# Kernel optimization log

Hardware: AMD Instinct MI355X
Metric: run time of the kernel (lower is better)

Reference implementation:

```python
import jax, jax.numpy as jnp
import numpy as np

INPUT, HIDDEN, OUTPUT = 512, 512, 512


def setup_inputs() -> dict:
    key = jax.random.key(0)
    ks = jax.random.split(key, 8)
    B, T = 64, 1024
    s_x = 1.0 / np.sqrt(INPUT)
    s_h = 1.0 / np.sqrt(HIDDEN)
    return {
        "x": jax.random.normal(ks[0], (B, T, INPUT), jnp.float32),
        "h0": jnp.zeros((B, HIDDEN), jnp.float32),
        # nn.Linear params: weight (out, in), bias (out,), U(-1/sqrt(in), 1/sqrt(in))
        "W_xh": jax.random.uniform(ks[1], (HIDDEN, INPUT), jnp.float32, -s_x, s_x),
        "b_xh": jax.random.uniform(ks[2], (HIDDEN,), jnp.float32, -s_x, s_x),
        "W_hh": jax.random.uniform(ks[3], (HIDDEN, HIDDEN), jnp.float32, -s_h, s_h),
        "b_hh": jax.random.uniform(ks[4], (HIDDEN,), jnp.float32, -s_h, s_h),
        "W_hy": jax.random.uniform(ks[5], (OUTPUT, HIDDEN), jnp.float32, -s_h, s_h),
        "b_hy": jax.random.uniform(ks[6], (OUTPUT,), jnp.float32, -s_h, s_h),
    }


def reference(x, h0, W_xh, b_xh, W_hh, b_hh, W_hy, b_hy):
    # h_t = tanh(W_hh h_{t-1} + b_hh + W_xh x_t + b_xh); y_t = W_hy h_t + b_hy
    # Precompute the input projection for all timesteps (one big GEMM).
    xp = jnp.einsum("bti,hi->bth", x, W_xh) + b_xh + b_hh  # (B, T, H)

    def step(h, xp_t):
        h = jnp.tanh(h @ W_hh.T + xp_t)
        return h, h

    h_n, hs = jax.lax.scan(step, h0, jnp.swapaxes(xp, 0, 1))  # hs: (T, B, H)
    hs = jnp.swapaxes(hs, 0, 1)  # (B, T, H)
    output = jnp.einsum("bth,oh->bto", hs, W_hy) + b_hy
    return output, h_n
```

## Files before the change

kernel.cpp:

```cpp
#include <hip/hip_runtime.h>

typedef _Float16 f16;
typedef _Float16 f16x2 __attribute__((ext_vector_type(2)));
typedef _Float16 f16x4 __attribute__((ext_vector_type(4)));
typedef _Float16 f16x8 __attribute__((ext_vector_type(8)));
typedef float    f32x4 __attribute__((ext_vector_type(4)));
typedef int      intx4 __attribute__((ext_vector_type(4)));


__global__ void cvt_f32_to_f16(const float* __restrict__ in, f16* __restrict__ out, int n) {
  int i = (blockIdx.x * blockDim.x + threadIdx.x) * 4;
  if (i + 3 < n) {
    float4 v = *(const float4*)(in + i);
    f16x4 h; h[0] = (f16)v.x; h[1] = (f16)v.y; h[2] = (f16)v.z; h[3] = (f16)v.w;
    *(f16x4*)(out + i) = h;
  }
}

__global__ void bias_comb_kernel(const float* __restrict__ a, const float* __restrict__ b,
                                 float* __restrict__ o, int n) {
  int i = blockIdx.x * blockDim.x + threadIdx.x;
  if (i < n) o[i] = a[i] + b[i];
}

__global__ void zero_u32_kernel(unsigned* p) { *p = 0u; }

__global__ void wabsmax_kernel(const float* __restrict__ in, int n, unsigned* out) {
  float m = 0.f;
  for (int i = blockIdx.x * blockDim.x + threadIdx.x; i < n; i += gridDim.x * blockDim.x)
    m = fmaxf(m, fabsf(in[i]));
#pragma unroll
  for (int off = 32; off >= 1; off >>= 1)
    m = fmaxf(m, __shfl_xor(m, off));
  if ((threadIdx.x & 63) == 0) atomicMax(out, __float_as_uint(m));
}

__global__ void quant_w_kernel(const float* __restrict__ W, signed char* __restrict__ out,
                               const unsigned* __restrict__ wmax, int n) {
  float mx = __uint_as_float(*wmax);
  float inv = mx > 0.f ? 127.f / mx : 0.f;
  int i = (blockIdx.x * blockDim.x + threadIdx.x) * 4;
  if (i + 3 < n) {
    float4 v = *(const float4*)(W + i);
    int q0 = (int)__builtin_rintf(v.x * inv);
    int q1 = (int)__builtin_rintf(v.y * inv);
    int q2 = (int)__builtin_rintf(v.z * inv);
    int q3 = (int)__builtin_rintf(v.w * inv);
    unsigned p = (unsigned)(q0 & 255) | ((unsigned)(q1 & 255) << 8) |
                 ((unsigned)(q2 & 255) << 16) | ((unsigned)(q3 & 255) << 24);
    *(unsigned*)(out + i) = p;
  }
}


#define BM 128
#define BN 128
#define BKT 32
#define LDK 40

template <bool A_IS_F32>
__global__ __launch_bounds__(256, 2) void gemm_f16_kernel(
    const void* __restrict__ Aptr,
    const f16* __restrict__ B,
    const float* __restrict__ bias,
    float* __restrict__ C,
    int M, int N, int K) {
  __shared__ f16 As[BM][LDK];
  __shared__ f16 Bs[BN][LDK];

  const int tid = threadIdx.x;
  const int bm = blockIdx.y, bn = blockIdx.x;
  const int wave = tid >> 6, lane = tid & 63;
  const int wm = wave >> 1, wn = wave & 1;

  f32x4 acc[4][4] = {};

  for (int k0 = 0; k0 < K; k0 += BKT) {
#pragma unroll
    for (int it = 0; it < 2; ++it) {
      int idx = tid + it * 256;
      int row = idx >> 2;
      int kc  = (idx & 3) << 3;
      if (A_IS_F32) {
        const float* Af = (const float*)Aptr + (size_t)(bm * BM + row) * K + k0 + kc;
        float4 v0 = *(const float4*)Af;
        float4 v1 = *(const float4*)(Af + 4);
        f16x8 h;
        h[0] = (f16)v0.x; h[1] = (f16)v0.y; h[2] = (f16)v0.z; h[3] = (f16)v0.w;
        h[4] = (f16)v1.x; h[5] = (f16)v1.y; h[6] = (f16)v1.z; h[7] = (f16)v1.w;
        *(f16x8*)&As[row][kc] = h;
      } else {
        const f16* Ah = (const f16*)Aptr + (size_t)(bm * BM + row) * K + k0 + kc;
        *(f16x8*)&As[row][kc] = *(const f16x8*)Ah;
      }
      const f16* Bh = B + (size_t)(bn * BN + row) * K + k0 + kc;
      *(f16x8*)&Bs[row][kc] = *(const f16x8*)Bh;
    }
    __syncthreads();

    const int fr = lane & 15;
    const int fk = (lane >> 4) << 3;
    f16x8 af[4], bf[4];
#pragma unroll
    for (int i = 0; i < 4; ++i) af[i] = *(const f16x8*)&As[wm * 64 + i * 16 + fr][fk];
#pragma unroll
    for (int j = 0; j < 4; ++j) bf[j] = *(const f16x8*)&Bs[wn * 64 + j * 16 + fr][fk];
#pragma unroll
    for (int i = 0; i < 4; ++i)
#pragma unroll
      for (int j = 0; j < 4; ++j)
        acc[i][j] = __builtin_amdgcn_mfma_f32_16x16x32_f16(af[i], bf[j], acc[i][j], 0, 0, 0);
    __syncthreads();
  }

  const int fr = lane & 15;
  const int fq = lane >> 4;
#pragma unroll
  for (int i = 0; i < 4; ++i)
#pragma unroll
    for (int j = 0; j < 4; ++j)
#pragma unroll
      for (int r = 0; r < 4; ++r) {
        int row = bm * BM + wm * 64 + i * 16 + fq * 4 + r;
        int col = bn * BN + wn * 64 + j * 16 + fr;
        C[(size_t)row * N + col] = acc[i][j][r] + bias[col];
      }
}


#define RT 512

#define MFMA(d, a, b) \
  asm("v_mfma_i32_16x16x64_i8 %0, %1, %2, %0" : "+v"(d) : "v"(a), "a"(b))

#define KSTEP2(s, Aeven, Bt0, Bt1, Bt2, Bt3) { \
    MFMA(Aeven##0, A##s, Bt0);                 \
    MFMA(Aeven##1, A##s, Bt1);                 \
    MFMA(Aeven##2, A##s, Bt2);                 \
    MFMA(Aeven##3, A##s, Bt3); }

#define BLD(s, nt) (*(const intx4*)(Whq + (size_t)(jb + (nt) * 16) * 512 + (s) * 64 + qoff))

__global__ __launch_bounds__(RT, 1) void rnn_scan_kernel(
    const signed char* __restrict__ Whq,
    const unsigned* __restrict__ wmax,
    const float* __restrict__ h0,
    const float* __restrict__ xp,
    f16* __restrict__ hs,
    float* __restrict__ hn,
    int T) {
  __shared__ __align__(64) signed char hbuf[2][RT];
  const int tid  = threadIdx.x;
  const int lane = tid & 63;
  const int w    = tid >> 6;
  const int b    = blockIdx.x;
  const int g    = lane >> 4;
  const int jb   = w * 64 + (lane & 15);
  const int j    = jb + g * 16;
  const int qoff = g << 4;

  const float qs = __uint_as_float(*wmax) * (1.0f / 16129.0f);

  intx4 B0_0=BLD(0,0), B0_1=BLD(0,1), B0_2=BLD(0,2), B0_3=BLD(0,3);
  intx4 B1_0=BLD(1,0), B1_1=BLD(1,1), B1_2=BLD(1,2), B1_3=BLD(1,3);
  intx4 B2_0=BLD(2,0), B2_1=BLD(2,1), B2_2=BLD(2,2), B2_3=BLD(2,3);
  intx4 B3_0=BLD(3,0), B3_1=BLD(3,1), B3_2=BLD(3,2), B3_3=BLD(3,3);
  intx4 B4_0=BLD(4,0), B4_1=BLD(4,1), B4_2=BLD(4,2), B4_3=BLD(4,3);
  intx4 B5_0=BLD(5,0), B5_1=BLD(5,1), B5_2=BLD(5,2), B5_3=BLD(5,3);
  intx4 B6_0=BLD(6,0), B6_1=BLD(6,1), B6_2=BLD(6,2), B6_3=BLD(6,3);
  intx4 B7_0=BLD(7,0), B7_1=BLD(7,1), B7_2=BLD(7,2), B7_3=BLD(7,3);

  {
    float hv = h0[(size_t)b * 512 + tid];
    hv = fminf(1.f, fmaxf(-1.f, hv));
    hbuf[0][tid] = (signed char)(int)__builtin_rintf(127.f * hv);
  }
  __syncthreads();

  const float* xpb = xp + (size_t)b * T * 512 + j;
  f16* hsb = hs + (size_t)b * T * 512 + j;

  int cur = 0;
  float hlast = 0.f;
  float xv = xpb[0];

  for (int t = 0; t < T; ++t) {
    int tn = t + 1 < T ? t + 1 : t;
    float xn = xpb[(size_t)tn * 512];

    const intx4* ap = (const intx4*)(&hbuf[cur][0] + qoff);
    intx4 A0 = ap[0],  A1 = ap[4],  A2 = ap[8],  A3 = ap[12],
          A4 = ap[16], A5 = ap[20], A6 = ap[24], A7 = ap[28];

    intx4 e0 = {0,0,0,0}, e1 = {0,0,0,0}, e2 = {0,0,0,0}, e3 = {0,0,0,0};
    intx4 o0 = {0,0,0,0}, o1 = {0,0,0,0}, o2 = {0,0,0,0}, o3 = {0,0,0,0};
    KSTEP2(0, e, B0_0, B0_1, B0_2, B0_3)
    KSTEP2(1, o, B1_0, B1_1, B1_2, B1_3)
    KSTEP2(2, e, B2_0, B2_1, B2_2, B2_3)
    KSTEP2(3, o, B3_0, B3_1, B3_2, B3_3)
    KSTEP2(4, e, B4_0, B4_1, B4_2, B4_3)
    KSTEP2(5, o, B5_0, B5_1, B5_2, B5_3)
    KSTEP2(6, e, B6_0, B6_1, B6_2, B6_3)
    KSTEP2(7, o, B7_0, B7_1, B7_2, B7_3)
    __builtin_amdgcn_sched_barrier(0);
    asm volatile("s_nop 7\ns_nop 7\ns_nop 7"
                 : "+v"(e0), "+v"(e1), "+v"(e2), "+v"(e3),
                   "+v"(o0), "+v"(o1), "+v"(o2), "+v"(o3));

    int s0 = e0[0] + o0[0];
    int s1 = e1[0] + o1[0];
    int s2 = e2[0] + o2[0];
    int s3 = e3[0] + o3[0];
    int slo = (g & 1) ? s1 : s0;
    int shi = (g & 1) ? s3 : s2;
    int sel = (g & 2) ? shi : slo;

    float y = (float)sel * qs + xv;
    float e = __expf(2.f * y);
    float hnew = 1.f - 2.f * __builtin_amdgcn_rcpf(e + 1.f);
    hlast = hnew;
    hsb[(size_t)t * 512] = (f16)hnew;
    hbuf[cur ^ 1][j] = (signed char)(int)__builtin_rintf(127.f * hnew);
    __syncthreads();
    cur ^= 1;
    xv = xn;
  }
  hn[(size_t)b * 512 + j] = hlast;
}


extern "C" void kernel_launch(void* const* d_in, const int* in_sizes, int n_in,
                              void* d_out, int out_size, void* d_ws, size_t ws_size,
                              hipStream_t stream) {
  const float* x    = (const float*)d_in[0];
  const float* h0   = (const float*)d_in[1];
  const float* W_xh = (const float*)d_in[2];
  const float* b_xh = (const float*)d_in[3];
  const float* W_hh = (const float*)d_in[4];
  const float* b_hh = (const float*)d_in[5];
  const float* W_hy = (const float*)d_in[6];
  const float* b_hy = (const float*)d_in[7];

  const int H = 512;
  const int B = in_sizes[1] / H;
  const int T = in_sizes[0] / (B * H);
  const int M = B * T;

  float* out = (float*)d_out;
  float* xpb = out;
  float* hn  = out + (size_t)M * H;

  char* w = (char*)d_ws;
  f16*         hsb    = (f16*)w;
  f16*         Wxh_h  = (f16*)(w + (size_t)M * H * 2);
  f16*         Why_h  = Wxh_h + H * H;
  signed char* Whq    = (signed char*)(Why_h + H * H);
  float*       biasc  = (float*)(Whq + H * H);
  unsigned*    wmax   = (unsigned*)(biasc + H);

  const int WN = H * H;
  cvt_f32_to_f16<<<WN / 1024, 256, 0, stream>>>(W_xh, Wxh_h, WN);
  cvt_f32_to_f16<<<WN / 1024, 256, 0, stream>>>(W_hy, Why_h, WN);
  bias_comb_kernel<<<2, 256, 0, stream>>>(b_xh, b_hh, biasc, H);

  zero_u32_kernel<<<1, 1, 0, stream>>>(wmax);
  wabsmax_kernel<<<64, 256, 0, stream>>>(W_hh, WN, wmax);
  quant_w_kernel<<<WN / 1024, 256, 0, stream>>>(W_hh, Whq, wmax, WN);

  gemm_f16_kernel<true><<<dim3(H / BN, M / BM), 256, 0, stream>>>(
      x, Wxh_h, biasc, xpb, M, H, H);

  rnn_scan_kernel<<<B, RT, 0, stream>>>(Whq, wmax, h0, xpb, hsb, hn, T);

  gemm_f16_kernel<false><<<dim3(H / BN, M / BM), 256, 0, stream>>>(
      hsb, Why_h, b_hy, out, M, H, H);
}
```

Measured before the change: 939.3 us.

## Halve scan block size, giving each wave 128 hidden units

Reduces the recurrent scan kernel to 4 waves per batch row, with each wave computing two 64-unit output groups using 8 independent MFMA accumulators per k-step. The goal is to reduce the per-timestep block barrier cost and drop the even/odd accumulator summation. In exchange each wave holds twice as many weight fragments in registers and issues twice as many serial MFMAs per step, which risks register pressure and longer per-step latency.

```diff
diff --git a/kernel.cpp b/kernel.cpp
--- a/kernel.cpp
+++ b/kernel.cpp
@@ -128,16 +128,20 @@
 }
 
 
-#define RT 512
+#define RT 256
 
 #define MFMA(d, a, b) \
   asm("v_mfma_i32_16x16x64_i8 %0, %1, %2, %0" : "+v"(d) : "v"(a), "a"(b))
 
-#define KSTEP2(s, Aeven, Bt0, Bt1, Bt2, Bt3) { \
-    MFMA(Aeven##0, A##s, Bt0);                 \
-    MFMA(Aeven##1, A##s, Bt1);                 \
-    MFMA(Aeven##2, A##s, Bt2);                 \
-    MFMA(Aeven##3, A##s, Bt3); }
+#define KSTEP(s) {                 \
+    MFMA(d0, A##s, B##s##_0);      \
+    MFMA(d1, A##s, B##s##_1);      \
+    MFMA(d2, A##s, B##s##_2);      \
+    MFMA(d3, A##s, B##s##_3);      \
+    MFMA(d4, A##s, B##s##_4);      \
+    MFMA(d5, A##s, B##s##_5);      \
+    MFMA(d6, A##s, B##s##_6);      \
+    MFMA(d7, A##s, B##s##_7); }
 
 #define BLD(s, nt) (*(const intx4*)(Whq + (size_t)(jb + (nt) * 16) * 512 + (s) * 64 + qoff))
 
@@ -149,83 +153,100 @@
     f16* __restrict__ hs,
     float* __restrict__ hn,
     int T) {
-  __shared__ __align__(64) signed char hbuf[2][RT];
+  __shared__ __align__(64) signed char hbuf[2][512];
   const int tid  = threadIdx.x;
   const int lane = tid & 63;
   const int w    = tid >> 6;
   const int b    = blockIdx.x;
   const int g    = lane >> 4;
-  const int jb   = w * 64 + (lane & 15);
-  const int j    = jb + g * 16;
+  const int jb   = w * 128 + (lane & 15);
+  const int j1   = jb + g * 16;
+  const int j2   = j1 + 64;
   const int qoff = g << 4;
 
   const float qs = __uint_as_float(*wmax) * (1.0f / 16129.0f);
 
-  intx4 B0_0=BLD(0,0), B0_1=BLD(0,1), B0_2=BLD(0,2), B0_3=BLD(0,3);
-  intx4 B1_0=BLD(1,0), B1_1=BLD(1,1), B1_2=BLD(1,2), B1_3=BLD(1,3);
-  intx4 B2_0=BLD(2,0), B2_1=BLD(2,1), B2_2=BLD(2,2), B2_3=BLD(2,3);
-  intx4 B3_0=BLD(3,0), B3_1=BLD(3,1), B3_2=BLD(3,2), B3_3=BLD(3,3);
-  intx4 B4_0=BLD(4,0), B4_1=BLD(4,1), B4_2=BLD(4,2), B4_3=BLD(4,3);
-  intx4 B5_0=BLD(5,0), B5_1=BLD(5,1), B5_2=BLD(5,2), B5_3=BLD(5,3);
-  intx4 B6_0=BLD(6,0), B6_1=BLD(6,1), B6_2=BLD(6,2), B6_3=BLD(6,3);
-  intx4 B7_0=BLD(7,0), B7_1=BLD(7,1), B7_2=BLD(7,2), B7_3=BLD(7,3);
+  intx4 B0_0=BLD(0,0), B0_1=BLD(0,1), B0_2=BLD(0,2), B0_3=BLD(0,3),
+        B0_4=BLD(0,4), B0_5=BLD(0,5), B0_6=BLD(0,6), B0_7=BLD(0,7);
+  intx4 B1_0=BLD(1,0), B1_1=BLD(1,1), B1_2=BLD(1,2), B1_3=BLD(1,3),
+        B1_4=BLD(1,4), B1_5=BLD(1,5), B1_6=BLD(1,6), B1_7=BLD(1,7);
+  intx4 B2_0=BLD(2,0), B2_1=BLD(2,1), B2_2=BLD(2,2), B2_3=BLD(2,3),
+        B2_4=BLD(2,4), B2_5=BLD(2,5), B2_6=BLD(2,6), B2_7=BLD(2,7);
+  intx4 B3_0=BLD(3,0), B3_1=BLD(3,1), B3_2=BLD(3,2), B3_3=BLD(3,3),
+        B3_4=BLD(3,4), B3_5=BLD(3,5), B3_6=BLD(3,6), B3_7=BLD(3,7);
+  intx4 B4_0=BLD(4,0), B4_1=BLD(4,1), B4_2=BLD(4,2), B4_3=BLD(4,3),
+        B4_4=BLD(4,4), B4_5=BLD(4,5), B4_6=BLD(4,6), B4_7=BLD(4,7);
+  intx4 B5_0=BLD(5,0), B5_1=BLD(5,1), B5_2=BLD(5,2), B5_3=BLD(5,3),
+        B5_4=BLD(5,4), B5_5=BLD(5,5), B5_6=BLD(5,6), B5_7=BLD(5,7);
+  intx4 B6_0=BLD(6,0), B6_1=BLD(6,1), B6_2=BLD(6,2), B6_3=BLD(6,3),
+        B6_4=BLD(6,4), B6_5=BLD(6,5), B6_6=BLD(6,6), B6_7=BLD(6,7);
+  intx4 B7_0=BLD(7,0), B7_1=BLD(7,1), B7_2=BLD(7,2), B7_3=BLD(7,3),
+        B7_4=BLD(7,4), B7_5=BLD(7,5), B7_6=BLD(7,6), B7_7=BLD(7,7);
 
   {
     float hv = h0[(size_t)b * 512 + tid];
     hv = fminf(1.f, fmaxf(-1.f, hv));
     hbuf[0][tid] = (signed char)(int)__builtin_rintf(127.f * hv);
+    float hv2 = h0[(size_t)b * 512 + tid + 256];
+    hv2 = fminf(1.f, fmaxf(-1.f, hv2));
+    hbuf[0][tid + 256] = (signed char)(int)__builtin_rintf(127.f * hv2);
   }
   __syncthreads();
 
-  const float* xpb = xp + (size_t)b * T * 512 + j;
-  f16* hsb = hs + (size_t)b * T * 512 + j;
+  const float* xpb1 = xp + (size_t)b * T * 512 + j1;
+  const float* xpb2 = xpb1 + 64;
+  f16* hsb1 = hs + (size_t)b * T * 512 + j1;
+  f16* hsb2 = hsb1 + 64;
 
   int cur = 0;
-  float hlast = 0.f;
-  float xv = xpb[0];
+  float hl1 = 0.f, hl2 = 0.f;
+  float xv1 = xpb1[0], xv2 = xpb2[0];
 
   for (int t = 0; t < T; ++t) {
     int tn = t + 1 < T ? t + 1 : t;
-    float xn = xpb[(size_t)tn * 512];
+    float xn1 = xpb1[(size_t)tn * 512];
+    float xn2 = xpb2[(size_t)tn * 512];
 
     const intx4* ap = (const intx4*)(&hbuf[cur][0] + qoff);
     intx4 A0 = ap[0],  A1 = ap[4],  A2 = ap[8],  A3 = ap[12],
           A4 = ap[16], A5 = ap[20], A6 = ap[24], A7 = ap[28];
 
-    intx4 e0 = {0,0,0,0}, e1 = {0,0,0,0}, e2 = {0,0,0,0}, e3 = {0,0,0,0};
-    intx4 o0 = {0,0,0,0}, o1 = {0,0,0,0}, o2 = {0,0,0,0}, o3 = {0,0,0,0};
-    KSTEP2(0, e, B0_0, B0_1, B0_2, B0_3)
-    KSTEP2(1, o, B1_0, B1_1, B1_2, B1_3)
-    KSTEP2(2, e, B2_0, B2_1, B2_2, B2_3)
-    KSTEP2(3, o, B3_0, B3_1, B3_2, B3_3)
-    KSTEP2(4, e, B4_0, B4_1, B4_2, B4_3)
-    KSTEP2(5, o, B5_0, B5_1, B5_2, B5_3)
-    KSTEP2(6, e, B6_0, B6_1, B6_2, B6_3)
-    KSTEP2(7, o, B7_0, B7_1, B7_2, B7_3)
+    intx4 d0 = {0,0,0,0}, d1 = {0,0,0,0}, d2 = {0,0,0,0}, d3 = {0,0,0,0},
+          d4 = {0,0,0,0}, d5 = {0,0,0,0}, d6 = {0,0,0,0}, d7 = {0,0,0,0};
+    KSTEP(0) KSTEP(1) KSTEP(2) KSTEP(3)
+    KSTEP(4) KSTEP(5) KSTEP(6) KSTEP(7)
     __builtin_amdgcn_sched_barrier(0);
     asm volatile("s_nop 7\ns_nop 7\ns_nop 7"
-                 : "+v"(e0), "+v"(e1), "+v"(e2), "+v"(e3),
-                   "+v"(o0), "+v"(o1), "+v"(o2), "+v"(o3));
-
-    int s0 = e0[0] + o0[0];
-    int s1 = e1[0] + o1[0];
-    int s2 = e2[0] + o2[0];
-    int s3 = e3[0] + o3[0];
-    int slo = (g & 1) ? s1 : s0;
-    int shi = (g & 1) ? s3 : s2;
-    int sel = (g & 2) ? shi : slo;
-
-    float y = (float)sel * qs + xv;
-    float e = __expf(2.f * y);
-    float hnew = 1.f - 2.f * __builtin_amdgcn_rcpf(e + 1.f);
-    hlast = hnew;
-    hsb[(size_t)t * 512] = (f16)hnew;
-    hbuf[cur ^ 1][j] = (signed char)(int)__builtin_rintf(127.f * hnew);
+                 : "+v"(d0), "+v"(d1), "+v"(d2), "+v"(d3),
+                   "+v"(d4), "+v"(d5), "+v"(d6), "+v"(d7));
+
+    int s0 = d0[0], s1 = d1[0], s2 = d2[0], s3 = d3[0];
+    int s4 = d4[0], s5 = d5[0], s6 = d6[0], s7 = d7[0];
+    int t01 = (g & 1) ? s1 : s0;
+    int t23 = (g & 1) ? s3 : s2;
+    int slo = (g & 2) ? t23 : t01;
+    int t45 = (g & 1) ? s5 : s4;
+    int t67 = (g & 1) ? s7 : s6;
+    int shi = (g & 2) ? t67 : t45;
+
+    float y1 = (float)slo * qs + xv1;
+    float y2 = (float)shi * qs + xv2;
+    float e1 = __expf(2.f * y1), e2 = __expf(2.f * y2);
+    float h1 = 1.f - 2.f * __builtin_amdgcn_rcpf(e1 + 1.f);
+    float h2 = 1.f - 2.f * __builtin_amdgcn_rcpf(e2 + 1.f);
+    hl1 = h1; hl2 = h2;
+    size_t ho = (size_t)t * 512;
+    hsb1[ho] = (f16)h1;
+    hsb2[ho] = (f16)h2;
+    signed char* hbw = hbuf[cur ^ 1];
+    hbw[j1] = (signed char)(int)__builtin_rintf(127.f * h1);
+    hbw[j2] = (signed char)(int)__builtin_rintf(127.f * h2);
     __syncthreads();
     cur ^= 1;
-    xv = xn;
-  }
-  hn[(size_t)b * 512 + j] = hlast;
+    xv1 = xn1; xv2 = xn2;
+  }
+  hn[(size_t)b * 512 + j1] = hl1;
+  hn[(size_t)b * 512 + j2] = hl2;
 }
 
 
```

Result: slower. 1.002 ms (+6.7%).
